# Kernel tuning notes

Measured on AMD Instinct MI355X. Metric: run time of the kernel, lower is better.

The kernel has to match this reference:

```python
import jax, jax.numpy as jnp
import numpy as np

EPS = 1e-4


def softmax_kernel(data, projection, is_query):
    # data: [b,h,n,d]; projection: [F,d]
    d = data.shape[-1]
    data_normalizer = d ** -0.25
    ratio = projection.shape[0] ** -0.5
    # [b,h,n,F]
    data_dash = jnp.einsum('bhnd,fd->bhnf', data_normalizer * data, projection)
    diag_data = (0.5 * (data_normalizer ** 2)) * jnp.sum(data * data, axis=-1, keepdims=True)
    if is_query:
        stab = jnp.max(data_dash, axis=-1, keepdims=True)
    else:
        stab = jnp.max(data_dash)
    return ratio * (jnp.exp(data_dash - diag_data - stab) + EPS)


def linear_attention(q, k, v):
    # q,k: [b,h,n,F]; v: [b,h,n,e]
    k_sum = k.sum(axis=-2)                                   # [b,h,F]
    d_inv = 1.0 / jnp.einsum('bhnf,bhf->bhn', q, k_sum)      # [b,h,n]
    context = jnp.einsum('bhnf,bhne->bhfe', k, v)            # [b,h,F,e]
    return jnp.einsum('bhfe,bhnf,bhn->bhne', context, q, d_inv)


def _gaussian_orthogonal_random_matrix(nb_rows, nb_cols, seed=0):
    # scaling=0: rows are orthogonal blocks rescaled by norms of iid gaussian rows
    rng = np.random.default_rng(seed)
    blocks = []
    full_blocks = nb_rows // nb_cols
    for _ in range(full_blocks):
        g = rng.standard_normal((nb_cols, nb_cols))
        qm, _ = np.linalg.qr(g)
        blocks.append(qm.T)
    rem = nb_rows - full_blocks * nb_cols
    if rem > 0:
        g = rng.standard_normal((nb_cols, nb_cols))
        qm, _ = np.linalg.qr(g)
        blocks.append(qm.T[:rem])
    mat = np.concatenate(blocks, axis=0)
    multiplier = np.linalg.norm(rng.standard_normal((nb_rows, nb_cols)), axis=1)
    return (multiplier[:, None] * mat).astype(np.float32)


def setup_inputs() -> dict:
    key = jax.random.key(0)
    kq, kk, kv = jax.random.split(key, 3)
    B, H, N, D = 2, 8, 8192, 64
    F = 256  # nb_features
    q = jax.random.normal(kq, (B, H, N, D), dtype=jnp.float32)
    k = jax.random.normal(kk, (B, H, N, D), dtype=jnp.float32)
    v = jax.random.normal(kv, (B, H, N, D), dtype=jnp.float32)
    projection = jnp.asarray(_gaussian_orthogonal_random_matrix(F, D, seed=0))
    return {"q": q, "k": k, "v": v, "projection": projection}


def reference(q, k, v, projection):
    qp = softmax_kernel(q, projection, is_query=True)
    kp = softmax_kernel(k, projection, is_query=False)
    return linear_attention(qp, kp, v)
```

## Files before the change

kernel.cpp:

```cpp
#include <hip/hip_runtime.h>


typedef __bf16 bf16;
typedef __bf16 bf16x8 __attribute__((ext_vector_type(8)));
typedef _Float16 f16;
typedef f16 f16x8 __attribute__((ext_vector_type(8)));
typedef float f32x4 __attribute__((ext_vector_type(4)));

#define N_    8192
#define BH_   16
#define NRM   0.35355339059327379f
#define RATIO 0.0625f
#define DSC   0.0625f
#define REPS  6.25e-6f

#define CTX_W  16
#define KSUM_W (CTX_W + BH_*256*64)
#define ZERO_W (KSUM_W + BH_*256)
#define SLICE_W 16640
#define PART_W  ZERO_W

static __device__ __forceinline__ unsigned mapmax(float x){
  unsigned u=__float_as_uint(x); return (u&0x80000000u)? ~u : (u|0x80000000u);
}
static __device__ __forceinline__ float unmapmax(unsigned u){
  return __uint_as_float((u&0x80000000u)? (u&0x7fffffffu) : ~u);
}
static __device__ __forceinline__ f32x4 mfma16(bf16x8 a, bf16x8 b, f32x4 c){
  return __builtin_amdgcn_mfma_f32_16x16x32_bf16(a,b,c,0,0,0);
}
static __device__ __forceinline__ f32x4 mfma16h(f16x8 a, f16x8 b, f32x4 c){
  return __builtin_amdgcn_mfma_f32_16x16x32_f16(a,b,c,0,0,0);
}
template<int CTRL>
static __device__ __forceinline__ float dppf(float x){
  int v=__builtin_amdgcn_update_dpp(0, __float_as_int(x), CTRL, 0xF, 0xF, true);
  return __int_as_float(v);
}
static __device__ __forceinline__ float max16_dpp(float x){
  x=fmaxf(x,dppf<0xB1>(x));
  x=fmaxf(x,dppf<0x4E>(x));
  x=fmaxf(x,dppf<0x141>(x));
  x=fmaxf(x,dppf<0x140>(x));
  return x;
}
static __device__ __forceinline__ float sum16_dpp(float x){
  x+=dppf<0xB1>(x);
  x+=dppf<0x4E>(x);
  x+=dppf<0x141>(x);
  x+=dppf<0x140>(x);
  return x;
}
static __device__ __forceinline__ void ld8(const float* __restrict__ p, float* x){
  float4 a=*(const float4*)p; float4 b=*(const float4*)(p+4);
  x[0]=a.x; x[1]=a.y; x[2]=a.z; x[3]=a.w; x[4]=b.x; x[5]=b.y; x[6]=b.z; x[7]=b.w;
}
static __device__ __forceinline__ void split8(const float* x, bf16x8& h, bf16x8& l){
  #pragma unroll
  for(int i=0;i<8;++i){ bf16 hi=(bf16)x[i]; h[i]=hi; l[i]=(bf16)(x[i]-(float)hi); }
}
static __device__ __forceinline__ void cvt8b(const float* x, bf16x8& h){
  #pragma unroll
  for(int i=0;i<8;++i) h[i]=(bf16)x[i];
}
static __device__ __forceinline__ void cvt8h(const float* x, f16x8& h){
  #pragma unroll
  for(int i=0;i<8;++i) h[i]=(f16)x[i];
}
static __device__ __forceinline__ void gload16(const float* g, float* l){
  __builtin_amdgcn_global_load_lds(
      (const __attribute__((address_space(1))) unsigned*)g,
      (__attribute__((address_space(3))) unsigned*)l, 16, 0, 0);
}
static __device__ __forceinline__ void load_P_frags1(const float* __restrict__ Pg,
    int fb, int l15, int g, bf16x8 (&pb)[4][2]){
  #pragma unroll
  for(int ft=0;ft<4;++ft)
    #pragma unroll
    for(int ks=0;ks<2;++ks){
      float x[8]; ld8(&Pg[(fb+16*ft+l15)*64+32*ks+8*g],x);
      #pragma unroll
      for(int i=0;i<8;++i) x[i]*=NRM;
      cvt8b(x,pb[ft][ks]);
    }
}

#define STAGE32(Xg, bufptr, n0s) do{                                      \
    int u0_=tid, u1_=tid+256;                                             \
    int r0_=u0_>>4, c0_=u0_&15, r1_=u1_>>4, c1_=u1_&15;                   \
    gload16((Xg)+((n0s)+r0_)*64+((c0_^(r0_&15))<<2), (bufptr)+u0_*4);     \
    gload16((Xg)+((n0s)+r1_)*64+((c1_^(r1_&15))<<2), (bufptr)+u1_*4);     \
  }while(0)
#define STAGE64(Xg, bufptr, n0s) do{                                      \
    _Pragma("unroll")                                                     \
    for(int ii_=0;ii_<4;++ii_){                                           \
      int u_=tid+256*ii_;                                                 \
      int r_=u_>>4, c_=u_&15;                                             \
      gload16((Xg)+((n0s)+r_)*64+((c_^(r_&15))<<2), (bufptr)+u_*4);       \
    }                                                                     \
  }while(0)
#define FRAGREAD(xv, bufptr, rr, ksv) do{                                 \
    int cc0_=(8*(ksv)+2*g)^((rr)&15);                                     \
    int cc1_=cc0_^1;                                                      \
    float4 a_=*(const float4*)((bufptr)+(rr)*64+cc0_*4);                  \
    float4 b_=*(const float4*)((bufptr)+(rr)*64+cc1_*4);                  \
    xv[0]=a_.x; xv[1]=a_.y; xv[2]=a_.z; xv[3]=a_.w;                       \
    xv[4]=b_.x; xv[5]=b_.y; xv[6]=b_.z; xv[7]=b_.w;                       \
  }while(0)


__global__ void __launch_bounds__(256) initK(unsigned* ws, int n){
  for(int i=blockIdx.x*256+threadIdx.x;i<n;i+=gridDim.x*256) ws[i]=0u;
}

__global__ void __launch_bounds__(256) stabK(const float* __restrict__ Kg,
                                             const float* __restrict__ Pg,
                                             unsigned* __restrict__ stab_ws){
  __shared__ float red[4];
  int tid=threadIdx.x, w=tid>>6, lane=tid&63, l15=lane&15, g=lane>>4;
  int fb=w*64;
  f16x8 pb[4][2];
  #pragma unroll
  for(int ft=0;ft<4;++ft)
    #pragma unroll
    for(int ks=0;ks<2;++ks){
      float x[8]; ld8(&Pg[(fb+16*ft+l15)*64+32*ks+8*g],x);
      #pragma unroll
      for(int i=0;i<8;++i) x[i]*=NRM;
      cvt8h(x,pb[ft][ks]);
    }
  float m=-3.4e38f;
  long base=(long)blockIdx.x*256;
  f32x4 zero={0.f,0.f,0.f,0.f};
  #pragma unroll 1
  for(int it=0;it<4;++it){
    long row0=base+it*64;
    f16x8 ka[4][2];
    #pragma unroll
    for(int rt=0;rt<4;++rt)
      #pragma unroll
      for(int ks=0;ks<2;++ks){
        float x[8]; ld8(&Kg[(row0+16*rt+l15)*64+32*ks+8*g],x);
        cvt8h(x,ka[rt][ks]);
      }
    f32x4 acc[4][4];
    #pragma unroll
    for(int rt=0;rt<4;++rt)
      #pragma unroll
      for(int ft=0;ft<4;++ft) acc[rt][ft]=zero;
    #pragma unroll
    for(int rt=0;rt<4;++rt)
      #pragma unroll
      for(int ft=0;ft<4;++ft)
        #pragma unroll
        for(int ks=0;ks<2;++ks)
          acc[rt][ft]=mfma16h(ka[rt][ks],pb[ft][ks],acc[rt][ft]);
    #pragma unroll
    for(int rt=0;rt<4;++rt)
      #pragma unroll
      for(int ft=0;ft<4;++ft)
        #pragma unroll
        for(int r=0;r<4;++r) m=fmaxf(m,acc[rt][ft][r]);
  }
  #pragma unroll
  for(int off=1;off<64;off<<=1) m=fmaxf(m,__shfl_xor(m,off));
  if(lane==0) red[w]=m;
  __syncthreads();
  if(tid==0){
    m=fmaxf(fmaxf(red[0],red[1]),fmaxf(red[2],red[3]));
    atomicMax(stab_ws,mapmax(m));
  }
}

__global__ void __launch_bounds__(256,2) ctxK(const float* __restrict__ Kg,
    const float* __restrict__ Vg, const float* __restrict__ Pg,
    const unsigned* __restrict__ stab_ws, float* __restrict__ ctx_g,
    float* __restrict__ ksum_g, float* __restrict__ part, int mode){
  __shared__ __align__(16) bf16 kpt_h[256*40];
  __shared__ float kstage[2][2048];
  int tid=threadIdx.x, w=tid>>6, lane=tid&63, l15=lane&15, g=lane>>4;
  int fb=w*64;
  int bh=blockIdx.x>>5, ch=blockIdx.x&31;
  long rowbase=(long)bh*N_ + ch*256;
  float stab=unmapmax(*stab_ws);
  bf16x8 pb[4][2];
  load_P_frags1(Pg,fb,l15,g,pb);
  f32x4 zero={0.f,0.f,0.f,0.f};
  f32x4 cacc[4][4];
  #pragma unroll
  for(int mt=0;mt<4;++mt)
    #pragma unroll
    for(int et=0;et<4;++et) cacc[mt][et]=zero;
  float ksacc[4]={0.f,0.f,0.f,0.f};
  int cur=0;
  STAGE32(Kg, &kstage[0][0], rowbase);
  __syncthreads();
  #pragma unroll 1
  for(int it=0;it<8;++it){
    long n0=rowbase+it*32;
    long np=(it==7)? rowbase : n0+32;
    STAGE32(Kg, &kstage[cur^1][0], np);
    float vx[4][8];
    #pragma unroll
    for(int et=0;et<4;++et)
      #pragma unroll
      for(int j=0;j<8;++j) vx[et][j]=Vg[(n0+8*g+j)*64+16*et+l15];
    bf16x8 ka[2][2];
    float dsq[2];
    #pragma unroll
    for(int rt=0;rt<2;++rt){
      float ss=0.f;
      #pragma unroll
      for(int ks=0;ks<2;++ks){
        float x[8]; FRAGREAD(x,&kstage[cur][0],16*rt+l15,ks);
        #pragma unroll
        for(int i=0;i<8;++i) ss=fmaf(x[i],x[i],ss);
        cvt8b(x,ka[rt][ks]);
      }
      ss+=__shfl_xor(ss,16); ss+=__shfl_xor(ss,32);
      dsq[rt]=DSC*ss;
    }
    f32x4 dacc[2][4];
    #pragma unroll
    for(int rt=0;rt<2;++rt)
      #pragma unroll
      for(int ft=0;ft<4;++ft) dacc[rt][ft]=zero;
    __builtin_amdgcn_s_setprio(1);
    #pragma unroll
    for(int rt=0;rt<2;++rt)
      #pragma unroll
      for(int ft=0;ft<4;++ft)
        #pragma unroll
        for(int ks=0;ks<2;++ks)
          dacc[rt][ft]=mfma16(ka[rt][ks],pb[ft][ks],dacc[rt][ft]);
    __builtin_amdgcn_s_setprio(0);
    float dg[2][4];
    #pragma unroll
    for(int rt=0;rt<2;++rt)
      #pragma unroll
      for(int r=0;r<4;++r) dg[rt][r]=__shfl(dsq[rt],4*g+r);
    #pragma unroll
    for(int rt=0;rt<2;++rt)
      #pragma unroll
      for(int ft=0;ft<4;++ft){
        int f=fb+16*ft+l15;
        ushort4 pk;
        unsigned short hvb[4];
        #pragma unroll
        for(int r=0;r<4;++r){
          float kp=fmaf(RATIO,__expf(dacc[rt][ft][r]-dg[rt][r]-stab),REPS);
          bf16 hb=(bf16)kp;
          ksacc[ft]+=(float)hb;
          hvb[r]=__builtin_bit_cast(unsigned short,hb);
        }
        pk.x=hvb[0]; pk.y=hvb[1]; pk.z=hvb[2]; pk.w=hvb[3];
        *(ushort4*)&kpt_h[f*40+16*rt+4*g]=pk;
      }
    bf16x8 vb_h[4], vb_l[4];
    #pragma unroll
    for(int et=0;et<4;++et) split8(vx[et],vb_h[et],vb_l[et]);
    __builtin_amdgcn_s_setprio(1);
    #pragma unroll
    for(int mt=0;mt<4;++mt){
      bf16x8 a_h=*(const bf16x8*)&kpt_h[(fb+16*mt+l15)*40+8*g];
      #pragma unroll
      for(int et=0;et<4;++et){
        cacc[mt][et]=mfma16(a_h,vb_h[et],cacc[mt][et]);
        cacc[mt][et]=mfma16(a_h,vb_l[et],cacc[mt][et]);
      }
    }
    __builtin_amdgcn_s_setprio(0);
    __syncthreads();
    cur^=1;
  }
  float ksred[4];
  #pragma unroll
  for(int ft=0;ft<4;++ft){
    float s=ksacc[ft];
    s+=__shfl_xor(s,16); s+=__shfl_xor(s,32);
    ksred[ft]=s;
  }
  if(mode){
    float* cg=part+((long)ch*BH_+bh)*SLICE_W;
    #pragma unroll
    for(int mt=0;mt<4;++mt)
      #pragma unroll
      for(int et=0;et<4;++et)
        #pragma unroll
        for(int r=0;r<4;++r)
          cg[(fb+16*mt+4*g+r)*64+16*et+l15]=cacc[mt][et][r];
    if(g==0){
      #pragma unroll
      for(int ft=0;ft<4;++ft)
        cg[16384+fb+16*ft+l15]=ksred[ft];
    }
  }else{
    float* cg=ctx_g+(long)bh*16384;
    #pragma unroll
    for(int mt=0;mt<4;++mt)
      #pragma unroll
      for(int et=0;et<4;++et)
        #pragma unroll
        for(int r=0;r<4;++r)
          atomicAdd(&cg[(fb+16*mt+4*g+r)*64+16*et+l15],cacc[mt][et][r]);
    if(g==0){
      #pragma unroll
      for(int ft=0;ft<4;++ft)
        atomicAdd(&ksum_g[bh*256+fb+16*ft+l15],ksred[ft]);
    }
  }
}

__global__ void __launch_bounds__(256) redK(const float* __restrict__ part,
    float* __restrict__ ctx_g, float* __restrict__ ksum_g){
  long t=(long)blockIdx.x*256+threadIdx.x;
  const long TOT=(long)BH_*SLICE_W;
  for(long o=t;o<TOT;o+=(long)gridDim.x*256){
    int bh=(int)(o/SLICE_W), idx=(int)(o%SLICE_W);
    float s=0.f;
    #pragma unroll 8
    for(int ch=0;ch<32;++ch)
      s+=part[((long)ch*BH_+bh)*SLICE_W+idx];
    if(idx<16384) ctx_g[(long)bh*16384+idx]=s;
    else          ksum_g[bh*256+idx-16384]=s;
  }
}

__global__ void __launch_bounds__(256,2) qoK(const float* __restrict__ Qg,
    const float* __restrict__ Pg, const float* __restrict__ ctx_g,
    const float* __restrict__ ksum_g, float* __restrict__ outg){
  __shared__ float qstage[2][4096];
  __shared__ __align__(16) bf16 qpt[64*264];
  __shared__ float rmaxl[4][64];
  __shared__ float denl[4][64];
  int tid=threadIdx.x, w=tid>>6, lane=tid&63, l15=lane&15, g=lane>>4;
  int fb=w*64;
  int bh=blockIdx.x>>5, ch=blockIdx.x&31;
  long rowbase=(long)bh*N_ + ch*256;

  bf16x8 pb[4][2];
  load_P_frags1(Pg,fb,l15,g,pb);
  float ksv[4];
  #pragma unroll
  for(int ft=0;ft<4;++ft) ksv[ft]=ksum_g[bh*256+fb+16*ft+l15];
  bf16x8 cb_h[8], cb_l[8];
  #pragma unroll
  for(int ks=0;ks<8;++ks){
    float x[8];
    #pragma unroll
    for(int j=0;j<8;++j) x[j]=ctx_g[(long)bh*16384+(32*ks+8*g+j)*64+16*w+l15];
    split8(x,cb_h[ks],cb_l[ks]);
  }
  f32x4 zero={0.f,0.f,0.f,0.f};
  int cur=0;
  STAGE64(Qg, &qstage[0][0], rowbase);
  __syncthreads();
  #pragma unroll 1
  for(int it=0;it<4;++it){
    long n0=rowbase+it*64;
    long np=(it==3)? rowbase : n0+64;
    STAGE64(Qg, &qstage[cur^1][0], np);
    f32x4 dacc[4][4];
    float dsq[4];
    #pragma unroll
    for(int rt=0;rt<4;++rt){
      bf16x8 qa[2];
      float ss=0.f;
      #pragma unroll
      for(int ks=0;ks<2;++ks){
        float x[8]; FRAGREAD(x,&qstage[cur][0],16*rt+l15,ks);
        #pragma unroll
        for(int i=0;i<8;++i) ss=fmaf(x[i],x[i],ss);
        cvt8b(x,qa[ks]);
      }
      ss+=__shfl_xor(ss,16); ss+=__shfl_xor(ss,32);
      dsq[rt]=DSC*ss;
      #pragma unroll
      for(int ft=0;ft<4;++ft) dacc[rt][ft]=zero;
      __builtin_amdgcn_s_setprio(1);
      #pragma unroll
      for(int ft=0;ft<4;++ft)
        #pragma unroll
        for(int ks=0;ks<2;++ks)
          dacc[rt][ft]=mfma16(qa[ks],pb[ft][ks],dacc[rt][ft]);
      __builtin_amdgcn_s_setprio(0);
    }
    float dg[4][4];
    #pragma unroll
    for(int rt=0;rt<4;++rt)
      #pragma unroll
      for(int r=0;r<4;++r) dg[rt][r]=__shfl(dsq[rt],4*g+r);
    #pragma unroll
    for(int rt=0;rt<4;++rt)
      #pragma unroll
      for(int r=0;r<4;++r){
        float m=fmaxf(fmaxf(dacc[rt][0][r],dacc[rt][1][r]),
                      fmaxf(dacc[rt][2][r],dacc[rt][3][r]));
        m=max16_dpp(m);
        if(l15==0) rmaxl[w][16*rt+4*g+r]=m;
      }
    __syncthreads();
    #pragma unroll
    for(int rt=0;rt<4;++rt)
      #pragma unroll
      for(int r=0;r<4;++r){
        int nn=16*rt+4*g+r;
        float rm=fmaxf(fmaxf(rmaxl[0][nn],rmaxl[1][nn]),
                       fmaxf(rmaxl[2][nn],rmaxl[3][nn]));
        float dp=0.f;
        #pragma unroll
        for(int ft=0;ft<4;++ft){
          float qp=fmaf(RATIO,__expf(dacc[rt][ft][r]-dg[rt][r]-rm),REPS);
          bf16 hb=(bf16)qp;
          dp=fmaf((float)hb,ksv[ft],dp);
          qpt[nn*264 + fb+16*ft+l15]=hb;
        }
        dp=sum16_dpp(dp);
        if(l15==0) denl[w][nn]=dp;
      }
    __syncthreads();
    f32x4 oacc[4];
    #pragma unroll
    for(int mt=0;mt<4;++mt) oacc[mt]=zero;
    __builtin_amdgcn_s_setprio(1);
    #pragma unroll
    for(int ks=0;ks<8;++ks)
      #pragma unroll
      for(int mt=0;mt<4;++mt){
        bf16x8 a_h=*(const bf16x8*)&qpt[(16*mt+l15)*264+32*ks+8*g];
        oacc[mt]=mfma16(a_h,cb_h[ks],oacc[mt]);
        oacc[mt]=mfma16(a_h,cb_l[ks],oacc[mt]);
      }
    __builtin_amdgcn_s_setprio(0);
    #pragma unroll
    for(int mt=0;mt<4;++mt)
      #pragma unroll
      for(int r=0;r<4;++r){
        int nn=16*mt+4*g+r;
        float den=denl[0][nn]+denl[1][nn]+denl[2][nn]+denl[3][nn];
        float rden=__builtin_amdgcn_rcpf(den);
        outg[(n0+nn)*64+16*w+l15]=oacc[mt][r]*rden;
      }
    cur^=1;
  }
}


extern "C" void kernel_launch(void* const* d_in, const int* in_sizes, int n_in,
                              void* d_out, int out_size, void* d_ws, size_t ws_size,
                              hipStream_t stream) {
  (void)in_sizes; (void)n_in; (void)out_size;
  const float* q = (const float*)d_in[0];
  const float* k = (const float*)d_in[1];
  const float* v = (const float*)d_in[2];
  const float* P = (const float*)d_in[3];
  float* out = (float*)d_out;

  unsigned* stab = (unsigned*)d_ws;
  float* ctx  = (float*)d_ws + CTX_W;
  float* ksum = (float*)d_ws + KSUM_W;
  float* part = (float*)d_ws + PART_W;

  size_t need = ((size_t)PART_W + (size_t)32*BH_*SLICE_W) * 4;
  int mode = (ws_size >= need) ? 1 : 0;

  if(mode)
    hipLaunchKernelGGL(initK, dim3(1), dim3(256), 0, stream, (unsigned*)d_ws, CTX_W);
  else
    hipLaunchKernelGGL(initK, dim3(256), dim3(256), 0, stream, (unsigned*)d_ws, ZERO_W);
  hipLaunchKernelGGL(stabK, dim3(512), dim3(256), 0, stream, k, P, stab);
  hipLaunchKernelGGL(ctxK, dim3(512), dim3(256), 0, stream, k, v, P, stab,
                     ctx, ksum, part, mode);
  if(mode)
    hipLaunchKernelGGL(redK, dim3(1040), dim3(256), 0, stream, part, ctx, ksum);
  hipLaunchKernelGGL(qoK, dim3(512), dim3(256), 0, stream, q, P, ctx, ksum, out);
}
```

Baseline: 110.8 us.

## Transpose Q-projection MFMA output so each lane owns one row's features

```diff
diff --git a/kernel.cpp b/kernel.cpp
--- a/kernel.cpp
+++ b/kernel.cpp
@@ -31,25 +31,6 @@
 }
 static __device__ __forceinline__ f32x4 mfma16h(f16x8 a, f16x8 b, f32x4 c){
   return __builtin_amdgcn_mfma_f32_16x16x32_f16(a,b,c,0,0,0);
-}
-template<int CTRL>
-static __device__ __forceinline__ float dppf(float x){
-  int v=__builtin_amdgcn_update_dpp(0, __float_as_int(x), CTRL, 0xF, 0xF, true);
-  return __int_as_float(v);
-}
-static __device__ __forceinline__ float max16_dpp(float x){
-  x=fmaxf(x,dppf<0xB1>(x));
-  x=fmaxf(x,dppf<0x4E>(x));
-  x=fmaxf(x,dppf<0x141>(x));
-  x=fmaxf(x,dppf<0x140>(x));
-  return x;
-}
-static __device__ __forceinline__ float sum16_dpp(float x){
-  x+=dppf<0xB1>(x);
-  x+=dppf<0x4E>(x);
-  x+=dppf<0x141>(x);
-  x+=dppf<0x140>(x);
-  return x;
 }
 static __device__ __forceinline__ void ld8(const float* __restrict__ p, float* x){
   float4 a=*(const float4*)p; float4 b=*(const float4*)(p+4);
@@ -340,9 +321,10 @@
 
   bf16x8 pb[4][2];
   load_P_frags1(Pg,fb,l15,g,pb);
-  float ksv[4];
-  #pragma unroll
-  for(int ft=0;ft<4;++ft) ksv[ft]=ksum_g[bh*256+fb+16*ft+l15];
+  float4 ksv2[4];
+  #pragma unroll
+  for(int ft=0;ft<4;++ft)
+    ksv2[ft]=*(const float4*)&ksum_g[bh*256+fb+16*ft+4*g];
   bf16x8 cb_h[8], cb_l[8];
   #pragma unroll
   for(int ks=0;ks<8;++ks){
@@ -382,42 +364,45 @@
       for(int ft=0;ft<4;++ft)
         #pragma unroll
         for(int ks=0;ks<2;++ks)
-          dacc[rt][ft]=mfma16(qa[ks],pb[ft][ks],dacc[rt][ft]);
+          dacc[rt][ft]=mfma16(pb[ft][ks],qa[ks],dacc[rt][ft]);
       __builtin_amdgcn_s_setprio(0);
     }
-    float dg[4][4];
-    #pragma unroll
-    for(int rt=0;rt<4;++rt)
-      #pragma unroll
-      for(int r=0;r<4;++r) dg[rt][r]=__shfl(dsq[rt],4*g+r);
-    #pragma unroll
-    for(int rt=0;rt<4;++rt)
-      #pragma unroll
-      for(int r=0;r<4;++r){
-        float m=fmaxf(fmaxf(dacc[rt][0][r],dacc[rt][1][r]),
-                      fmaxf(dacc[rt][2][r],dacc[rt][3][r]));
-        m=max16_dpp(m);
-        if(l15==0) rmaxl[w][16*rt+4*g+r]=m;
-      }
+    #pragma unroll
+    for(int rt=0;rt<4;++rt){
+      float m=-3.4e38f;
+      #pragma unroll
+      for(int ft=0;ft<4;++ft)
+        #pragma unroll
+        for(int r=0;r<4;++r) m=fmaxf(m,dacc[rt][ft][r]);
+      m=fmaxf(m,__shfl_xor(m,16));
+      m=fmaxf(m,__shfl_xor(m,32));
+      if(g==0) rmaxl[w][16*rt+l15]=m;
+    }
     __syncthreads();
     #pragma unroll
-    for(int rt=0;rt<4;++rt)
-      #pragma unroll
-      for(int r=0;r<4;++r){
-        int nn=16*rt+4*g+r;
-        float rm=fmaxf(fmaxf(rmaxl[0][nn],rmaxl[1][nn]),
-                       fmaxf(rmaxl[2][nn],rmaxl[3][nn]));
-        float dp=0.f;
-        #pragma unroll
-        for(int ft=0;ft<4;++ft){
-          float qp=fmaf(RATIO,__expf(dacc[rt][ft][r]-dg[rt][r]-rm),REPS);
+    for(int rt=0;rt<4;++rt){
+      int nn=16*rt+l15;
+      float rm=fmaxf(fmaxf(rmaxl[0][nn],rmaxl[1][nn]),
+                     fmaxf(rmaxl[2][nn],rmaxl[3][nn]));
+      float base=dsq[rt]+rm;
+      float dp=0.f;
+      #pragma unroll
+      for(int ft=0;ft<4;++ft){
+        unsigned short hvb[4];
+        float kw[4]={ksv2[ft].x,ksv2[ft].y,ksv2[ft].z,ksv2[ft].w};
+        #pragma unroll
+        for(int r=0;r<4;++r){
+          float qp=fmaf(RATIO,__expf(dacc[rt][ft][r]-base),REPS);
           bf16 hb=(bf16)qp;
-          dp=fmaf((float)hb,ksv[ft],dp);
-          qpt[nn*264 + fb+16*ft+l15]=hb;
+          dp=fmaf((float)hb,kw[r],dp);
+          hvb[r]=__builtin_bit_cast(unsigned short,hb);
         }
-        dp=sum16_dpp(dp);
-        if(l15==0) denl[w][nn]=dp;
-      }
+        ushort4 pk; pk.x=hvb[0]; pk.y=hvb[1]; pk.z=hvb[2]; pk.w=hvb[3];
+        *(ushort4*)&qpt[nn*264 + fb+16*ft+4*g]=pk;
+      }
+      dp+=__shfl_xor(dp,16); dp+=__shfl_xor(dp,32);
+      if(g==0) denl[w][nn]=dp;
+    }
     __syncthreads();
     f32x4 oacc[4];
     #pragma unroll
```

After: 105.8 us. 4.5% less time.
